# Performance work log

Hardware: AMD Instinct MI355X
Metric: run time of the kernel (lower is better)

The kernel has to match this reference:

```python
import jax, jax.numpy as jnp
import numpy as np

N = 131072   # total nodes in batch
E = 524288   # directed edges
B = 2048     # number of graphs
H = 128      # hidden_dim
NF = 30      # node_feature_dim
GF = 4415    # gene_feature_dim
L = 3        # gnn_layers
EPS = 1e-5   # batchnorm eps


def setup_inputs() -> dict:
    key = jax.random.key(0)
    ks = jax.random.split(key, 24)
    rn = lambda k, s, sc=0.05: jax.random.normal(k, s, jnp.float32) * sc
    return {
        "x": jax.random.normal(ks[0], (N, NF), jnp.float32),
        "gene_features": jax.random.normal(ks[1], (B, GF), jnp.float32),
        "edge_index": jax.random.randint(ks[2], (2, E), 0, N),
        "batch": (jnp.arange(N) * B) // N,  # sorted, every graph non-empty
        "W_emb": rn(ks[3], (NF, H)), "b_emb": jnp.zeros((H,), jnp.float32),
        "Wg": rn(ks[4], (L, H, H)), "bg": jnp.zeros((L, H), jnp.float32),
        "bn_gamma": jnp.ones((L, H), jnp.float32), "bn_beta": jnp.zeros((L, H), jnp.float32),
        "Wd1": rn(ks[5], (2 * H, H)), "bd1": jnp.zeros((H,), jnp.float32),
        "Wd2": rn(ks[6], (H, H)), "bd2": jnp.zeros((H,), jnp.float32),
        "Wge1": rn(ks[7], (GF, 256)), "bge1": jnp.zeros((256,), jnp.float32),
        "g_gamma": jnp.ones((256,), jnp.float32), "g_beta": jnp.zeros((256,), jnp.float32),
        "Wge2": rn(ks[8], (256, H)), "bge2": jnp.zeros((H,), jnp.float32),
        "Wh1": rn(ks[9], (2 * H, H)), "bh1": jnp.zeros((H,), jnp.float32),
        "h_gamma": jnp.ones((H,), jnp.float32), "h_beta": jnp.zeros((H,), jnp.float32),
        "Wh2": rn(ks[10], (H, 64)), "bh2": jnp.zeros((64,), jnp.float32),
        "Wh3": rn(ks[11], (64, 1)), "bh3": jnp.zeros((1,), jnp.float32),
    }


def _bn_eval(x, gamma, beta):
    # inference batchnorm with running_mean=0, running_var=1
    return x * (gamma / jnp.sqrt(1.0 + EPS)) + beta


def _gcn_conv(h, W, b, src, dst):
    # PyG GCNConv: add self-loops, symmetric deg normalization, W first, bias after agg
    hw = h @ W                                            # [N,H]
    loop = jnp.arange(N)
    src_a = jnp.concatenate([src, loop])                  # [E+N]
    dst_a = jnp.concatenate([dst, loop])
    deg = jax.ops.segment_sum(jnp.ones((E + N,), hw.dtype), dst_a, num_segments=N)
    dinv = jnp.where(deg > 0, jax.lax.rsqrt(deg), 0.0)
    norm = dinv[src_a] * dinv[dst_a]                      # [E+N]
    msgs = hw[src_a] * norm[:, None]                      # gather [E+N,H]
    out = jax.ops.segment_sum(msgs, dst_a, num_segments=N)
    return out + b


def reference(x, gene_features, edge_index, batch, W_emb, b_emb, Wg, bg, bn_gamma,
              bn_beta, Wd1, bd1, Wd2, bd2, Wge1, bge1, g_gamma, g_beta, Wge2, bge2,
              Wh1, bh1, h_gamma, h_beta, Wh2, bh2, Wh3, bh3):
    src, dst = edge_index[0], edge_index[1]
    h = jax.nn.relu(x @ W_emb + b_emb)                    # [N,H]
    for i in range(L):
        hn = _gcn_conv(h, Wg[i], bg[i], src, dst)
        hn = jax.nn.relu(_bn_eval(hn, bn_gamma[i], bn_beta[i]))
        h = hn if i == 0 else h + hn                      # residual for i>0
    # global mean / max pooling per graph
    counts = jax.ops.segment_sum(jnp.ones((N,), h.dtype), batch, num_segments=B)
    mean_pool = jax.ops.segment_sum(h, batch, num_segments=B) / jnp.maximum(counts, 1.0)[:, None]
    max_pool = jax.ops.segment_max(h, batch, num_segments=B)
    graph_repr = jnp.concatenate([mean_pool, max_pool], axis=1)   # [B,2H]
    drug = jax.nn.relu(graph_repr @ Wd1 + bd1) @ Wd2 + bd2        # [B,H]
    g1 = jax.nn.relu(_bn_eval(gene_features @ Wge1 + bge1, g_gamma, g_beta))
    gene = jax.nn.relu(g1 @ Wge2 + bge2)                          # [B,H]
    comb = jnp.concatenate([drug, gene], axis=1)                  # [B,2H]
    z = jax.nn.relu(_bn_eval(comb @ Wh1 + bh1, h_gamma, h_beta))
    z = jax.nn.relu(z @ Wh2 + bh2)
    return z @ Wh3 + bh3                                          # [B,1]
```

## Files before the change

kernel.cpp:

```cpp
#include <hip/hip_runtime.h>

#define N_NODES 131072
#define E_EDGES 524288
#define B_GR    2048
#define H_DIM   128
#define NF_DIM  30
#define GF_DIM  4415
#define GF_PAD  4416
#define BN_SCALE 0.9999950000374997f
#define NSPLIT  32

typedef __bf16 bf16x8 __attribute__((ext_vector_type(8)));
typedef float  f32x4  __attribute__((ext_vector_type(4)));
typedef unsigned int uint32;
typedef uint32 u32x4 __attribute__((ext_vector_type(4)));

__device__ __forceinline__ void split2(float x, __bf16& hi, __bf16& lo){
    hi = (__bf16)x;
    lo = (__bf16)(x - (float)hi);
}
__device__ __forceinline__ uint32 bfbits(float x){
    __bf16 h = (__bf16)x;
    return (uint32)__builtin_bit_cast(unsigned short, h);
}
__device__ __forceinline__ float unpack_even(uint32 u){ return __uint_as_float(u<<16); }
__device__ __forceinline__ float unpack_odd (uint32 u){ return __uint_as_float(u & 0xffff0000u); }
__device__ __forceinline__ uint32 pack2(float e, float o){ return bfbits(e) | (bfbits(o)<<16); }


__global__ void k_zero2(int* __restrict__ a, int na, float* __restrict__ b, int nb){
    int i = blockIdx.x*256 + threadIdx.x;
    if(i < na) a[i] = 0;
    int j = i - na;
    if(j >= 0 && j < nb) b[j] = 0.f;
}

__global__ void k_count(const int* __restrict__ dst, int* __restrict__ counts){
    int e = blockIdx.x*256 + threadIdx.x;
    if(e < E_EDGES) atomicAdd(&counts[dst[e]], 1);
}

__global__ void k_scan1(int* __restrict__ counts, int* __restrict__ bsums){
    __shared__ int s[1024];
    int t = threadIdx.x;
    int gi = blockIdx.x*1024 + t;
    int v = counts[gi];
    s[t] = v; __syncthreads();
    for(int off=1; off<1024; off<<=1){
        int x = (t>=off) ? s[t-off] : 0;
        __syncthreads();
        s[t] += x;
        __syncthreads();
    }
    counts[gi] = s[t] - v;
    if(t == 1023) bsums[blockIdx.x] = s[t];
}

__global__ void k_scan2(int* __restrict__ bsums){
    __shared__ int s[128];
    int t = threadIdx.x;
    int v = bsums[t]; s[t] = v; __syncthreads();
    for(int off=1; off<128; off<<=1){
        int x = (t>=off) ? s[t-off] : 0;
        __syncthreads();
        s[t] += x;
        __syncthreads();
    }
    bsums[t] = s[t] - v;
}

__global__ void k_scan3(const int* __restrict__ counts, const int* __restrict__ bsums,
                        int* __restrict__ rowptr, float* __restrict__ dinv,
                        int* __restrict__ cursor){
    int i = blockIdx.x*1024 + threadIdx.x;
    int r0 = counts[i] + bsums[blockIdx.x];
    int r1;
    if(i == N_NODES-1){
        r1 = E_EDGES;
        rowptr[N_NODES] = E_EDGES;
    } else {
        int ip = i + 1;
        int nb = (threadIdx.x == 1023) ? blockIdx.x + 1 : blockIdx.x;
        r1 = counts[ip] + bsums[nb];
    }
    rowptr[i] = r0;
    dinv[i] = rsqrtf((float)(r1 - r0) + 1.0f);
    cursor[i] = r0;
}

__global__ void k_fill(const int* __restrict__ src, const int* __restrict__ dst,
                       int* __restrict__ cursor, int* __restrict__ csr){
    int e = blockIdx.x*256 + threadIdx.x;
    if(e < E_EDGES){
        int p = atomicAdd(&cursor[dst[e]], 1);
        csr[p] = src[e];
    }
}


__global__ void k_split_weights(const float* __restrict__ Wge1, __bf16* __restrict__ wth,
                                __bf16* __restrict__ wtl,
                                const float* __restrict__ Wg, __bf16* __restrict__ gth,
                                __bf16* __restrict__ gtl,
                                const float* __restrict__ Wemb, __bf16* __restrict__ eth,
                                __bf16* __restrict__ etl){
    __shared__ float sTile[64][65];
    unsigned bid = blockIdx.x;
    int tid = threadIdx.x;
    if(bid < 276u){
        int kt = bid % 69u, ct = bid / 69u;
        int k0 = kt*64, c0 = ct*64;
        #pragma unroll
        for(int i=0;i<16;i++){
            int idx = i*256 + tid;
            int kk = idx >> 6, cc = idx & 63;
            int k = k0 + kk;
            sTile[kk][cc] = (k < GF_DIM) ? Wge1[(size_t)k*256 + c0 + cc] : 0.f;
        }
        __syncthreads();
        #pragma unroll
        for(int i=0;i<16;i++){
            int idx = i*256 + tid;
            int cc = idx >> 6, kk = idx & 63;
            float v = sTile[kk][cc];
            size_t o = (size_t)(c0 + cc)*GF_PAD + k0 + kk;
            split2(v, wth[o], wtl[o]);
        }
    } else if(bid < 276u + 192u){
        int idx = (bid - 276u)*256 + tid;
        int l = idx >> 14, i = idx & 16383;
        int k = i >> 7, c = i & 127;
        float v = Wg[idx];
        int o = (l << 14) + (c << 7) + k;
        split2(v, gth[o], gtl[o]);
    } else {
        int idx = (bid - 468u)*256 + tid;
        int c = idx >> 5, k = idx & 31;
        float v = (k < NF_DIM) ? Wemb[k*H_DIM + c] : 0.f;
        split2(v, eth[idx], etl[idx]);
    }
}


__global__ __launch_bounds__(256)
void k_emb_mfma(const float* __restrict__ x,
                const __bf16* __restrict__ wth, const __bf16* __restrict__ wtl,
                const float* __restrict__ bias, uint32* __restrict__ Hh2,
                uint32* __restrict__ Hl2){
    __shared__ float sT[4][32*68];
    int wave = threadIdx.x >> 6, lane = threadIdx.x & 63;
    int lr = lane & 15, lq = lane >> 4;
    int rbase = blockIdx.x*128 + wave*32;
    const f32x4 zero4 = {0.f,0.f,0.f,0.f};
    const float* xr0 = x + (size_t)(rbase + lr)*NF_DIM;
    const float* xr1 = x + (size_t)(rbase + 16 + lr)*NF_DIM;
    bf16x8 A0h, A0l, A1h, A1l;
    #pragma unroll
    for(int t=0;t<8;t++){
        int k = lq*8 + t;
        float v0 = (k < NF_DIM) ? xr0[k] : 0.f;
        float v1 = (k < NF_DIM) ? xr1[k] : 0.f;
        __bf16 h, l;
        split2(v0, h, l); A0h[t] = h; A0l[t] = l;
        split2(v1, h, l); A1h[t] = h; A1l[t] = l;
    }
    int orow = lane >> 3;
    int oq   = lane & 7;
    float* sW = sT[wave];
    for(int ph=0; ph<2; ph++){
        #pragma unroll
        for(int cc=0; cc<4; cc++){
            int col = (ph*4+cc)*16 + lr;
            bf16x8 Bh = *(const bf16x8*)(wth + col*32 + lq*8);
            bf16x8 Bl = *(const bf16x8*)(wtl + col*32 + lq*8);
            f32x4 a0 = zero4, a1 = zero4;
            a0 = __builtin_amdgcn_mfma_f32_16x16x32_bf16(A0h, Bh, a0, 0,0,0);
            a0 = __builtin_amdgcn_mfma_f32_16x16x32_bf16(A0l, Bh, a0, 0,0,0);
            a0 = __builtin_amdgcn_mfma_f32_16x16x32_bf16(A0h, Bl, a0, 0,0,0);
            a1 = __builtin_amdgcn_mfma_f32_16x16x32_bf16(A1h, Bh, a1, 0,0,0);
            a1 = __builtin_amdgcn_mfma_f32_16x16x32_bf16(A1l, Bh, a1, 0,0,0);
            a1 = __builtin_amdgcn_mfma_f32_16x16x32_bf16(A1h, Bl, a1, 0,0,0);
            #pragma unroll
            for(int r=0;r<4;r++){
                sW[(lq*4+r)*68 + cc*16 + lr]    = a0[r];
                sW[(16+lq*4+r)*68 + cc*16 + lr] = a1[r];
            }
        }
        __syncthreads();
        int cg = ph*64 + oq*8;
        float bb[8];
        *(float4*)&bb[0] = *(const float4*)(bias + cg);
        *(float4*)&bb[4] = *(const float4*)(bias + cg + 4);
        #pragma unroll
        for(int i=0;i<4;i++){
            int row = i*8 + orow;
            float v[8];
            *(float4*)&v[0] = *(float4*)&sW[row*68 + oq*8];
            *(float4*)&v[4] = *(float4*)&sW[row*68 + oq*8 + 4];
            uint32 oh[4], ol[4];
            #pragma unroll
            for(int p=0;p<4;p++){
                float ve = fmaxf(v[2*p]   + bb[2*p],   0.f);
                float vo = fmaxf(v[2*p+1] + bb[2*p+1], 0.f);
                uint32 he = bfbits(ve), ho = bfbits(vo);
                oh[p] = he | (ho<<16);
                float le = ve - __uint_as_float(he<<16);
                float lo = vo - __uint_as_float(ho<<16);
                ol[p] = pack2(le, lo);
            }
            size_t oidx = (size_t)(rbase + row)*64 + (cg>>1);
            *(uint4*)(Hh2 + oidx) = make_uint4(oh[0],oh[1],oh[2],oh[3]);
            *(uint4*)(Hl2 + oidx) = make_uint4(ol[0],ol[1],ol[2],ol[3]);
        }
        __syncthreads();
    }
}


struct MetaA {
    int   j0A, cA, j0B, cB;
    float dnA, dnB;
    uint32 shA, slA, shB, slB;
};

__device__ __forceinline__ void load_metaA(MetaA& m, int nA, int lane,
                                           const int* __restrict__ rowptr,
                                           const float* __restrict__ dinv,
                                           const uint32* __restrict__ Hh2,
                                           const uint32* __restrict__ Hl2){
    int nB = nA + 8;
    int a0 = rowptr[nA], a1 = rowptr[nA+1];
    int b0 = rowptr[nB], b1 = rowptr[nB+1];
    m.j0A = a0; m.cA = a1 - a0;
    m.j0B = b0; m.cB = b1 - b0;
    m.dnA = dinv[nA]; m.dnB = dinv[nB];
    size_t iA = (size_t)nA*64 + lane, iB = (size_t)nB*64 + lane;
    m.shA = Hh2[iA]; m.slA = Hl2[iA];
    m.shB = Hh2[iB]; m.slB = Hl2[iB];
}

__device__ __forceinline__ void load_jj(int* jjA, int* jjB, const MetaA& m,
                                        const int* __restrict__ csr){
    int jmA = m.j0A + m.cA - 1;
    int jmB = m.j0B + m.cB - 1;
    #pragma unroll
    for(int t=0;t<8;t++){
        int ia = m.j0A + t; ia = ia > jmA ? jmA : ia;
        int ib = m.j0B + t; ib = ib > jmB ? jmB : ib;
        jjA[t] = csr[ia] & (N_NODES-1);
        jjB[t] = csr[ib] & (N_NODES-1);
    }
}

__device__ __forceinline__ void agg_step(
        const MetaA& cur, const int* jjA, const int* jjB, int ii,
        MetaA* m2, int n2,
        int* jj1A, int* jj1B, const MetaA* m1,
        int base16, int lane,
        const uint32* __restrict__ Hh2, const uint32* __restrict__ Hl2,
        const float* __restrict__ dinv, const int* __restrict__ rowptr,
        const int* __restrict__ csr,
        uint32* __restrict__ AhL, uint32* __restrict__ AlL){
    uint32 rrA[8], rrB[8];
    float  wwA[8], wwB[8];
    #pragma unroll
    for(int t=0;t<8;t++){
        wwA[t] = (t < cur.cA) ? dinv[jjA[t]] : 0.f;
        rrA[t] = Hh2[(size_t)jjA[t]*64 + lane];
        wwB[t] = (t < cur.cB) ? dinv[jjB[t]] : 0.f;
        rrB[t] = Hh2[(size_t)jjB[t]*64 + lane];
    }
    if(m2) load_metaA(*m2, n2, lane, rowptr, dinv, Hh2, Hl2);
    if(m1) load_jj(jj1A, jj1B, *m1, csr);
    float axA = (unpack_even(cur.shA) + unpack_even(cur.slA)) * cur.dnA;
    float ayA = (unpack_odd(cur.shA)  + unpack_odd(cur.slA))  * cur.dnA;
    float axB = (unpack_even(cur.shB) + unpack_even(cur.slB)) * cur.dnB;
    float ayB = (unpack_odd(cur.shB)  + unpack_odd(cur.slB))  * cur.dnB;
    #pragma unroll
    for(int t=0;t<8;t++){
        axA = fmaf(unpack_even(rrA[t]), wwA[t], axA);
        ayA = fmaf(unpack_odd(rrA[t]),  wwA[t], ayA);
        axB = fmaf(unpack_even(rrB[t]), wwB[t], axB);
        ayB = fmaf(unpack_odd(rrB[t]),  wwB[t], ayB);
    }
    int nb = cur.cA > cur.cB ? cur.cA : cur.cB;
    if(nb > 8){
        int jmA = cur.j0A + cur.cA - 1;
        int jmB = cur.j0B + cur.cB - 1;
        for(int j=8; j<nb; j+=8){
            int jja[8], jjb[8]; float wa[8], wb[8]; uint32 ra[8], rb[8];
            #pragma unroll
            for(int t=0;t<8;t++){
                int ia = cur.j0A + j + t; ia = ia > jmA ? jmA : ia;
                int ib = cur.j0B + j + t; ib = ib > jmB ? jmB : ib;
                jja[t] = csr[ia] & (N_NODES-1);
                jjb[t] = csr[ib] & (N_NODES-1);
            }
            #pragma unroll
            for(int t=0;t<8;t++){
                wa[t] = (j + t < cur.cA) ? dinv[jja[t]] : 0.f;
                ra[t] = Hh2[(size_t)jja[t]*64 + lane];
                wb[t] = (j + t < cur.cB) ? dinv[jjb[t]] : 0.f;
                rb[t] = Hh2[(size_t)jjb[t]*64 + lane];
            }
            #pragma unroll
            for(int t=0;t<8;t++){
                axA = fmaf(unpack_even(ra[t]), wa[t], axA);
                ayA = fmaf(unpack_odd(ra[t]),  wa[t], ayA);
                axB = fmaf(unpack_even(rb[t]), wb[t], axB);
                ayB = fmaf(unpack_odd(rb[t]),  wb[t], ayB);
            }
        }
    }
    axA *= cur.dnA; ayA *= cur.dnA;
    axB *= cur.dnB; ayB *= cur.dnB;
    int rowA = base16 + ii, rowB = rowA + 8;
    uint32 hxA = bfbits(axA), hyA = bfbits(ayA);
    AhL[rowA*68 + lane] = hxA | (hyA<<16);
    AlL[rowA*68 + lane] = pack2(axA - __uint_as_float(hxA<<16),
                                ayA - __uint_as_float(hyA<<16));
    uint32 hxB = bfbits(axB), hyB = bfbits(ayB);
    AhL[rowB*68 + lane] = hxB | (hyB<<16);
    AlL[rowB*68 + lane] = pack2(axB - __uint_as_float(hxB<<16),
                                ayB - __uint_as_float(hyB<<16));
}

__global__ __launch_bounds__(512, 4)
void k_layer(const __bf16* __restrict__ curHh, const __bf16* __restrict__ curHl,
             const float* __restrict__ dinv, const int* __restrict__ rowptr,
             const int* __restrict__ csr,
             const __bf16* __restrict__ Bth, const __bf16* __restrict__ Btl,
             const float* __restrict__ bias, const float* __restrict__ gamma,
             const float* __restrict__ beta,
             uint32* __restrict__ outHh2, uint32* __restrict__ outHl2, int residual){
    __shared__ uint32 smem[8*32*68];
    uint32* AhL = smem;
    uint32* AlL = smem + 128*68;
    int tid  = threadIdx.x;
    int wave = __builtin_amdgcn_readfirstlane(tid >> 6);
    int lane = tid & 63;
    int rbase = blockIdx.x * 128;
    int base16 = wave*16;
    const uint32* Hh2 = (const uint32*)curHh;
    const uint32* Hl2 = (const uint32*)curHl;

    {
        MetaA m0, m1, m2;
        int jj0A[8], jj0B[8], jj1A[8], jj1B[8];
        int nb0 = rbase + base16;
        load_metaA(m0, nb0+0, lane, rowptr, dinv, Hh2, Hl2);
        load_metaA(m1, nb0+1, lane, rowptr, dinv, Hh2, Hl2);
        load_jj(jj0A, jj0B, m0, csr);
        agg_step(m0, jj0A, jj0B, 0, &m2, nb0+2, jj1A, jj1B, &m1,
                 base16, lane, Hh2, Hl2, dinv, rowptr, csr, AhL, AlL);
        agg_step(m1, jj1A, jj1B, 1, &m0, nb0+3, jj0A, jj0B, &m2,
                 base16, lane, Hh2, Hl2, dinv, rowptr, csr, AhL, AlL);
        agg_step(m2, jj0A, jj0B, 2, &m1, nb0+4, jj1A, jj1B, &m0,
                 base16, lane, Hh2, Hl2, dinv, rowptr, csr, AhL, AlL);
        agg_step(m0, jj1A, jj1B, 3, &m2, nb0+5, jj0A, jj0B, &m1,
                 base16, lane, Hh2, Hl2, dinv, rowptr, csr, AhL, AlL);
        agg_step(m1, jj0A, jj0B, 4, &m0, nb0+6, jj1A, jj1B, &m2,
                 base16, lane, Hh2, Hl2, dinv, rowptr, csr, AhL, AlL);
        agg_step(m2, jj1A, jj1B, 5, &m1, nb0+7, jj0A, jj0B, &m0,
                 base16, lane, Hh2, Hl2, dinv, rowptr, csr, AhL, AlL);
        agg_step(m0, jj0A, jj0B, 6, nullptr, 0, jj1A, jj1B, &m1,
                 base16, lane, Hh2, Hl2, dinv, rowptr, csr, AhL, AlL);
        agg_step(m1, jj1A, jj1B, 7, nullptr, 0, nullptr, nullptr, nullptr,
                 base16, lane, Hh2, Hl2, dinv, rowptr, csr, AhL, AlL);
    }
    __syncthreads();

    int lr = lane & 15, lq = lane >> 4;
    int wr = wave & 3, wc = wave >> 2;
    int r0 = wr*32;
    bf16x8 A0h[4], A0l[4], A1h[4], A1l[4];
    #pragma unroll
    for(int ks=0;ks<4;ks++){
        int u0 = (r0 + lr)*68 + lq*4 + ks*16;
        int u1 = (r0 + 16 + lr)*68 + lq*4 + ks*16;
        A0h[ks] = __builtin_bit_cast(bf16x8, *(const u32x4*)(AhL + u0));
        A0l[ks] = __builtin_bit_cast(bf16x8, *(const u32x4*)(AlL + u0));
        A1h[ks] = __builtin_bit_cast(bf16x8, *(const u32x4*)(AhL + u1));
        A1l[ks] = __builtin_bit_cast(bf16x8, *(const u32x4*)(AlL + u1));
    }
    __syncthreads();

    float* stg = (float*)smem + wave*(32*68);
    const f32x4 zero4 = {0.f,0.f,0.f,0.f};
    #pragma unroll
    for(int cc=0; cc<4; cc++){
        int col = wc*64 + cc*16 + lr;
        f32x4 a0 = zero4, a1 = zero4;
        #pragma unroll
        for(int ks=0;ks<4;ks++){
            bf16x8 Bh = *(const bf16x8*)(Bth + col*H_DIM + ks*32 + lq*8);
            bf16x8 Bl = *(const bf16x8*)(Btl + col*H_DIM + ks*32 + lq*8);
            a0 = __builtin_amdgcn_mfma_f32_16x16x32_bf16(A0h[ks], Bh, a0, 0,0,0);
            a0 = __builtin_amdgcn_mfma_f32_16x16x32_bf16(A0l[ks], Bh, a0, 0,0,0);
            a0 = __builtin_amdgcn_mfma_f32_16x16x32_bf16(A0h[ks], Bl, a0, 0,0,0);
            a1 = __builtin_amdgcn_mfma_f32_16x16x32_bf16(A1h[ks], Bh, a1, 0,0,0);
            a1 = __builtin_amdgcn_mfma_f32_16x16x32_bf16(A1l[ks], Bh, a1, 0,0,0);
            a1 = __builtin_amdgcn_mfma_f32_16x16x32_bf16(A1h[ks], Bl, a1, 0,0,0);
        }
        #pragma unroll
        for(int r=0;r<4;r++){
            stg[(lq*4+r)*68 + cc*16 + lr]    = a0[r];
            stg[(16+lq*4+r)*68 + cc*16 + lr] = a1[r];
        }
    }

    int orow = lane >> 3;
    int oq   = lane & 7;
    int cg = wc*64 + oq*8;
    float bb[8], gg[8], tt[8];
    *(float4*)&bb[0] = *(const float4*)(bias + cg);
    *(float4*)&bb[4] = *(const float4*)(bias + cg + 4);
    *(float4*)&gg[0] = *(const float4*)(gamma + cg);
    *(float4*)&gg[4] = *(const float4*)(gamma + cg + 4);
    *(float4*)&tt[0] = *(const float4*)(beta + cg);
    *(float4*)&tt[4] = *(const float4*)(beta + cg + 4);
    #pragma unroll
    for(int p=0;p<8;p++) gg[p] *= BN_SCALE;
    #pragma unroll
    for(int i=0;i<4;i++){
        int row = i*8 + orow;
        float v[8];
        *(float4*)&v[0] = *(float4*)&stg[row*68 + oq*8];
        *(float4*)&v[4] = *(float4*)&stg[row*68 + oq*8 + 4];
        size_t oidx = (size_t)(rbase + r0 + row)*64 + (cg>>1);
        uint4 oldh = {0,0,0,0}, oldl = {0,0,0,0};
        if(residual){
            oldh = *(const uint4*)(Hh2 + oidx);
            oldl = *(const uint4*)(Hl2 + oidx);
        }
        uint32 ohv[4] = {oldh.x,oldh.y,oldh.z,oldh.w};
        uint32 olv[4] = {oldl.x,oldl.y,oldl.z,oldl.w};
        uint32 oh[4], ol[4];
        #pragma unroll
        for(int p=0;p<4;p++){
            float ve = fmaxf(fmaf(v[2*p]   + bb[2*p],   gg[2*p],   tt[2*p]),   0.f);
            float vo = fmaxf(fmaf(v[2*p+1] + bb[2*p+1], gg[2*p+1], tt[2*p+1]), 0.f);
            if(residual){
                ve += unpack_even(ohv[p]) + unpack_even(olv[p]);
                vo += unpack_odd(ohv[p])  + unpack_odd(olv[p]);
            }
            uint32 he = bfbits(ve), ho = bfbits(vo);
            oh[p] = he | (ho<<16);
            float le = ve - __uint_as_float(he<<16);
            float lo = vo - __uint_as_float(ho<<16);
            ol[p] = pack2(le, lo);
        }
        *(uint4*)(outHh2 + oidx) = make_uint4(oh[0],oh[1],oh[2],oh[3]);
        *(uint4*)(outHl2 + oidx) = make_uint4(ol[0],ol[1],ol[2],ol[3]);
    }
}


__global__ __launch_bounds__(256)
void k_gemm_gf_mfma(const float* __restrict__ Agf,
                    const __bf16* __restrict__ Bth, const __bf16* __restrict__ Btl,
                    float* __restrict__ g1acc){
    int rt = blockIdx.x & 31;
    int sp = blockIdx.x >> 5;
    int ks0 = (sp*138) >> 5, ks1 = ((sp+1)*138) >> 5;
    int wave = threadIdx.x >> 6, lane = threadIdx.x & 63;
    int lr = lane & 15, lq = lane >> 4;
    int rbase = rt*64 + (wave & 1)*32;
    int cbase = (wave >> 1)*128;
    const f32x4 zero4 = {0.f,0.f,0.f,0.f};
    f32x4 acc[8][2];
    #pragma unroll
    for(int ct=0;ct<8;ct++){ acc[ct][0] = zero4; acc[ct][1] = zero4; }
    for(int ks=ks0; ks<ks1; ks++){
        int kc = ks*32;
        const float* ar0 = Agf + (size_t)(rbase + lr)*GF_DIM + kc + lq*8;
        const float* ar1 = ar0 + (size_t)16*GF_DIM;
        bf16x8 A0h, A0l, A1h, A1l;
        if(kc + 32 <= GF_DIM){
            #pragma unroll
            for(int t=0;t<8;t++){
                __bf16 h, l;
                split2(ar0[t], h, l); A0h[t] = h; A0l[t] = l;
                split2(ar1[t], h, l); A1h[t] = h; A1l[t] = l;
            }
        } else {
            #pragma unroll
            for(int t=0;t<8;t++){
                int k = kc + lq*8 + t;
                float v0 = 0.f, v1 = 0.f;
                if(k < GF_DIM){ v0 = ar0[t]; v1 = ar1[t]; }
                __bf16 h, l;
                split2(v0, h, l); A0h[t] = h; A0l[t] = l;
                split2(v1, h, l); A1h[t] = h; A1l[t] = l;
            }
        }
        #pragma unroll
        for(int ct=0;ct<8;ct++){
            size_t bo = (size_t)(cbase + ct*16 + lr)*GF_PAD + kc + lq*8;
            bf16x8 Bh = *(const bf16x8*)(Bth + bo);
            bf16x8 Bl = *(const bf16x8*)(Btl + bo);
            acc[ct][0] = __builtin_amdgcn_mfma_f32_16x16x32_bf16(A0h, Bh, acc[ct][0], 0,0,0);
            acc[ct][0] = __builtin_amdgcn_mfma_f32_16x16x32_bf16(A0l, Bh, acc[ct][0], 0,0,0);
            acc[ct][0] = __builtin_amdgcn_mfma_f32_16x16x32_bf16(A0h, Bl, acc[ct][0], 0,0,0);
            acc[ct][1] = __builtin_amdgcn_mfma_f32_16x16x32_bf16(A1h, Bh, acc[ct][1], 0,0,0);
            acc[ct][1] = __builtin_amdgcn_mfma_f32_16x16x32_bf16(A1l, Bh, acc[ct][1], 0,0,0);
            acc[ct][1] = __builtin_amdgcn_mfma_f32_16x16x32_bf16(A1h, Bl, acc[ct][1], 0,0,0);
        }
    }
    #pragma unroll
    for(int ct=0;ct<8;ct++)
        #pragma unroll
        for(int s=0;s<2;s++)
            #pragma unroll
            for(int r=0;r<4;r++)
                atomicAdd(&g1acc[(size_t)(rbase + s*16 + lq*4 + r)*256 + cbase + ct*16 + lr],
                          acc[ct][s][r]);
}


__device__ __forceinline__ void load_w4(const float* __restrict__ W, int off, int tid,
                                        float4* t){
    const float4* s = (const float4*)(W + off);
    t[0] = s[tid];
    t[1] = s[tid + 512];
    t[2] = s[tid + 1024];
    t[3] = s[tid + 1536];
}
__device__ __forceinline__ void write_w4(float* sW, int tid, const float4* t){
    float4* d = (float4*)sW;
    d[tid]        = t[0];
    d[tid + 512]  = t[1];
    d[tid + 1024] = t[2];
    d[tid + 1536] = t[3];
}

__device__ __forceinline__ void dense_stage128(
        const float* __restrict__ W, int nck, const float* sA, int lda,
        float* sO, int ldo, float* sW, int tid, int c, int ga, int gb,
        float bias_c, float gsc, float bsh, int do_relu){
    float4 t[4];
    load_w4(W, 0, tid, t);
    write_w4(sW, tid, t);
    __syncthreads();
    float a0 = bias_c, a1 = bias_c;
    for(int ck=0; ck<nck; ck++){
        if(ck+1 < nck) load_w4(W, (ck+1)*8192, tid, t);
        const float* aga = sA + ga*lda + ck*64;
        const float* agb = sA + gb*lda + ck*64;
        #pragma unroll
        for(int k=0;k<64;k++){
            float w = sW[k*128 + c];
            a0 = fmaf(aga[k], w, a0);
            a1 = fmaf(agb[k], w, a1);
        }
        __syncthreads();
        if(ck+1 < nck){ write_w4(sW, tid, t); __syncthreads(); }
    }
    a0 = fmaf(a0, gsc, bsh);
    a1 = fmaf(a1, gsc, bsh);
    if(do_relu){ a0 = fmaxf(a0, 0.f); a1 = fmaxf(a1, 0.f); }
    sO[ga*ldo + c] = a0;
    sO[gb*ldo + c] = a1;
}

__global__ __launch_bounds__(512)
void k_head(const uint32* __restrict__ Hh2, const uint32* __restrict__ Hl2,
            const float* __restrict__ g1acc,
            const float* __restrict__ bge1, const float* __restrict__ g_g,
            const float* __restrict__ g_b,
            const float* __restrict__ Wd1, const float* __restrict__ bd1,
            const float* __restrict__ Wd2, const float* __restrict__ bd2,
            const float* __restrict__ Wge2, const float* __restrict__ bge2,
            const float* __restrict__ Wh1, const float* __restrict__ bh1,
            const float* __restrict__ h_g, const float* __restrict__ h_b,
            const float* __restrict__ Wh2, const float* __restrict__ bh2,
            const float* __restrict__ Wh3, const float* __restrict__ bh3,
            float* __restrict__ out){
    __shared__ float sPool[8][256];
    __shared__ float sG1[8][256];
    __shared__ float sT1[8][128];
    __shared__ float sComb[8][256];
    __shared__ float sZ[8][128];
    __shared__ float sZ2[8][64];
    __shared__ float sW[8192];
    int tid = threadIdx.x;
    int wave = tid >> 6, lane = tid & 63;
    int g0 = blockIdx.x*8;
    {
        int idx = tid*4;
        int g = idx >> 8, c = idx & 255;
        float4 a  = *(const float4*)&g1acc[(size_t)(g0+g)*256 + c];
        float4 b  = *(const float4*)&bge1[c];
        float4 gm = *(const float4*)&g_g[c];
        float4 bt = *(const float4*)&g_b[c];
        sG1[g][c+0] = fmaxf(fmaf(a.x + b.x, gm.x*BN_SCALE, bt.x), 0.f);
        sG1[g][c+1] = fmaxf(fmaf(a.y + b.y, gm.y*BN_SCALE, bt.y), 0.f);
        sG1[g][c+2] = fmaxf(fmaf(a.z + b.z, gm.z*BN_SCALE, bt.z), 0.f);
        sG1[g][c+3] = fmaxf(fmaf(a.w + b.w, gm.w*BN_SCALE, bt.w), 0.f);
    }
    {
        size_t base = (size_t)(g0+wave)*4096 + lane;
        float se = 0.f, so = 0.f, me = -3.4e38f, mo = -3.4e38f;
        #pragma unroll 8
        for(int r=0;r<64;r++){
            uint32 h = Hh2[base + r*64];
            uint32 l = Hl2[base + r*64];
            float ve = unpack_even(h) + unpack_even(l);
            float vo = unpack_odd(h)  + unpack_odd(l);
            se += ve; so += vo;
            me = fmaxf(me, ve); mo = fmaxf(mo, vo);
        }
        sPool[wave][2*lane]       = se*(1.f/64.f);
        sPool[wave][2*lane+1]     = so*(1.f/64.f);
        sPool[wave][128+2*lane]   = me;
        sPool[wave][128+2*lane+1] = mo;
    }
    __syncthreads();
    int c = tid & 127, q = tid >> 7;
    int ga = 2*q, gb = 2*q + 1;
    dense_stage128(Wd1, 4, &sPool[0][0], 256, &sT1[0][0], 128, sW, tid, c, ga, gb,
                   bd1[c], 1.f, 0.f, 1);
    dense_stage128(Wd2, 2, &sT1[0][0], 128, &sComb[0][0], 256, sW, tid, c, ga, gb,
                   bd2[c], 1.f, 0.f, 0);
    dense_stage128(Wge2, 4, &sG1[0][0], 256, &sComb[0][0] + 128, 256, sW, tid, c, ga, gb,
                   bge2[c], 1.f, 0.f, 1);
    dense_stage128(Wh1, 4, &sComb[0][0], 256, &sZ[0][0], 128, sW, tid, c, ga, gb,
                   bh1[c], h_g[c]*BN_SCALE, h_b[c], 1);
    {
        float4 t[4];
        load_w4(Wh2, 0, tid, t);
        write_w4(sW, tid, t);
        __syncthreads();
        int c2 = tid & 63, q2 = tid >> 6;
        float a = bh2[c2];
        #pragma unroll
        for(int k=0;k<128;k++)
            a = fmaf(sZ[q2][k], sW[k*64 + c2], a);
        sZ2[q2][c2] = fmaxf(a, 0.f);
    }
    __syncthreads();
    {
        float v = sZ2[wave][lane] * Wh3[lane];
        #pragma unroll
        for(int off=32; off; off>>=1) v += __shfl_down(v, off);
        if(lane == 0) out[g0 + wave] = v + bh3[0];
    }
}


extern "C" void kernel_launch(void* const* d_in, const int* in_sizes, int n_in,
                              void* d_out, int out_size, void* d_ws, size_t ws_size,
                              hipStream_t stream){
    (void)in_sizes; (void)n_in; (void)out_size; (void)ws_size;
    const float* x    = (const float*)d_in[0];
    const float* gf   = (const float*)d_in[1];
    const int*   ei   = (const int*)  d_in[2];
    const float* W_emb= (const float*)d_in[4];
    const float* b_emb= (const float*)d_in[5];
    const float* Wg   = (const float*)d_in[6];
    const float* bg   = (const float*)d_in[7];
    const float* bn_g = (const float*)d_in[8];
    const float* bn_b = (const float*)d_in[9];
    const float* Wd1  = (const float*)d_in[10];
    const float* bd1  = (const float*)d_in[11];
    const float* Wd2  = (const float*)d_in[12];
    const float* bd2  = (const float*)d_in[13];
    const float* Wge1 = (const float*)d_in[14];
    const float* bge1 = (const float*)d_in[15];
    const float* g_g  = (const float*)d_in[16];
    const float* g_b  = (const float*)d_in[17];
    const float* Wge2 = (const float*)d_in[18];
    const float* bge2 = (const float*)d_in[19];
    const float* Wh1  = (const float*)d_in[20];
    const float* bh1  = (const float*)d_in[21];
    const float* h_g  = (const float*)d_in[22];
    const float* h_b  = (const float*)d_in[23];
    const float* Wh2  = (const float*)d_in[24];
    const float* bh2  = (const float*)d_in[25];
    const float* Wh3  = (const float*)d_in[26];
    const float* bh3  = (const float*)d_in[27];
    float* outp = (float*)d_out;

    char* base = (char*)d_ws;
    __bf16* Hh = (__bf16*)base;
    __bf16* Hl = (__bf16*)(base + (32u<<20));
    __bf16* Ph = (__bf16*)(base + (64u<<20));
    __bf16* Pl = (__bf16*)(base + (96u<<20));
    __bf16* wge_th = (__bf16*)(base + (64u<<20));
    __bf16* wge_tl = (__bf16*)(base + (64u<<20) + 2260992);
    char* T = base + (128u<<20);
    float* g1acc = (float*)T;
    int* counts = (int*)(g1acc + B_GR*256);
    int* rowptr = counts + N_NODES;
    int* cursor = rowptr + (N_NODES+1);
    int* csr    = cursor + N_NODES;
    int* bsums  = csr + E_EDGES;
    float* dinv = (float*)(bsums + 128);
    __bf16* wg_th = (__bf16*)(dinv + N_NODES);
    __bf16* wg_tl = wg_th + 3*16384;
    __bf16* we_th = wg_tl + 3*16384;
    __bf16* we_tl = we_th + 128*32;

    const int* src = ei;
    const int* dst = ei + E_EDGES;

    k_split_weights<<<484, 256, 0, stream>>>(Wge1, wge_th, wge_tl, Wg, wg_th, wg_tl,
                                             W_emb, we_th, we_tl);

    k_zero2<<<(N_NODES + B_GR*256 + 255)/256, 256, 0, stream>>>(counts, N_NODES,
                                                                g1acc, B_GR*256);

    k_gemm_gf_mfma<<<32*NSPLIT, 256, 0, stream>>>(gf, wge_th, wge_tl, g1acc);

    k_count<<<E_EDGES/256, 256, 0, stream>>>(dst, counts);
    k_scan1<<<128, 1024, 0, stream>>>(counts, bsums);
    k_scan2<<<1, 128, 0, stream>>>(bsums);
    k_scan3<<<128, 1024, 0, stream>>>(counts, bsums, rowptr, dinv, cursor);
    k_fill <<<E_EDGES/256, 256, 0, stream>>>(src, dst, cursor, csr);

    k_emb_mfma<<<N_NODES/128, 256, 0, stream>>>(x, we_th, we_tl, b_emb,
                                                (uint32*)Hh, (uint32*)Hl);

    uint32 *curh = (uint32*)Hh, *curl = (uint32*)Hl;
    uint32 *outh = (uint32*)Ph, *outl = (uint32*)Pl;
    for(int i=0;i<3;i++){
        k_layer<<<N_NODES/128, 512, 0, stream>>>((const __bf16*)curh, (const __bf16*)curl,
                                                 dinv, rowptr, csr,
                                                 wg_th + i*16384, wg_tl + i*16384,
                                                 bg + i*H_DIM, bn_g + i*H_DIM, bn_b + i*H_DIM,
                                                 outh, outl, i > 0);
        uint32* th = curh; curh = outh; outh = th;
        uint32* tl = curl; curl = outl; outl = tl;
    }

    k_head<<<B_GR/8, 512, 0, stream>>>(curh, curl, g1acc, bge1, g_g, g_b,
                                       Wd1, bd1, Wd2, bd2, Wge2, bge2,
                                       Wh1, bh1, h_g, h_b, Wh2, bh2, Wh3, bh3, outp);
}
```

Before: 583.0 us.

## Tile Wge1 weights per MFMA block, stage A via LDS, replace atomics with split-K reduce

The transposed, split Wge1 weights are repacked into contiguous 16x32 tiles, one per MFMA fragment, so B loads are dense. The gene-feature A tile is now loaded with coalesced float4 reads into shared memory before the bf16 split. Each split-K slice writes its partials to a scratch buffer, and a separate reduce kernel sums them, which replaces the float atomics and the zeroing of g1acc. The split count is halved to 16, which lowers reduce traffic but leaves fewer blocks in flight and adds a kernel launch.

Measured after the change: 582.8 us (median of 2 runs). Within noise of the previous version (-0.0%).

```diff
diff --git a/kernel.cpp b/kernel.cpp
--- a/kernel.cpp
+++ b/kernel.cpp
@@ -8,7 +8,7 @@
 #define GF_DIM  4415
 #define GF_PAD  4416
 #define BN_SCALE 0.9999950000374997f
-#define NSPLIT  32
+#define NSPLIT  16
 
 typedef __bf16 bf16x8 __attribute__((ext_vector_type(8)));
 typedef float  f32x4  __attribute__((ext_vector_type(4)));
@@ -28,11 +28,9 @@
 __device__ __forceinline__ uint32 pack2(float e, float o){ return bfbits(e) | (bfbits(o)<<16); }
 
 
-__global__ void k_zero2(int* __restrict__ a, int na, float* __restrict__ b, int nb){
+__global__ void k_zero_int(int* __restrict__ p, int n){
     int i = blockIdx.x*256 + threadIdx.x;
-    if(i < na) a[i] = 0;
-    int j = i - na;
-    if(j >= 0 && j < nb) b[j] = 0.f;
+    if(i < n) p[i] = 0;
 }
 
 __global__ void k_count(const int* __restrict__ dst, int* __restrict__ counts){
@@ -123,7 +121,8 @@
             int idx = i*256 + tid;
             int cc = idx >> 6, kk = idx & 63;
             float v = sTile[kk][cc];
-            size_t o = (size_t)(c0 + cc)*GF_PAD + k0 + kk;
+            int c = c0 + cc, k = k0 + kk;
+            size_t o = ((size_t)(c >> 4)*138 + (k >> 5))*512 + (c & 15)*32 + (k & 31);
             split2(v, wth[o], wtl[o]);
         }
     } else if(bid < 276u + 192u){
@@ -459,44 +458,54 @@
 __global__ __launch_bounds__(256)
 void k_gemm_gf_mfma(const float* __restrict__ Agf,
                     const __bf16* __restrict__ Bth, const __bf16* __restrict__ Btl,
-                    float* __restrict__ g1acc){
+                    float* __restrict__ gpart){
+    __shared__ float sA[64*34];
     int rt = blockIdx.x & 31;
     int sp = blockIdx.x >> 5;
-    int ks0 = (sp*138) >> 5, ks1 = ((sp+1)*138) >> 5;
-    int wave = threadIdx.x >> 6, lane = threadIdx.x & 63;
+    int ks0 = (sp*138) >> 4, ks1 = ((sp+1)*138) >> 4;
+    int tid = threadIdx.x;
+    int wave = tid >> 6, lane = tid & 63;
     int lr = lane & 15, lq = lane >> 4;
-    int rbase = rt*64 + (wave & 1)*32;
+    int rblk = rt*64;
+    int rhalf = (wave & 1)*32;
     int cbase = (wave >> 1)*128;
     const f32x4 zero4 = {0.f,0.f,0.f,0.f};
     f32x4 acc[8][2];
     #pragma unroll
     for(int ct=0;ct<8;ct++){ acc[ct][0] = zero4; acc[ct][1] = zero4; }
+    int srow = tid >> 2, sq = tid & 3;
     for(int ks=ks0; ks<ks1; ks++){
         int kc = ks*32;
-        const float* ar0 = Agf + (size_t)(rbase + lr)*GF_DIM + kc + lq*8;
-        const float* ar1 = ar0 + (size_t)16*GF_DIM;
+        __syncthreads();
+        {
+            int k0 = kc + sq*8;
+            const float* srcp = Agf + (size_t)(rblk + srow)*GF_DIM + k0;
+            float v[8];
+            if(k0 + 8 <= GF_DIM){
+                *(float4*)&v[0] = *(const float4*)srcp;
+                *(float4*)&v[4] = *(const float4*)(srcp + 4);
+            } else {
+                #pragma unroll
+                for(int t=0;t<8;t++) v[t] = (k0 + t < GF_DIM) ? srcp[t] : 0.f;
+            }
+            #pragma unroll
+            for(int t=0;t<8;t++) sA[srow*34 + sq*8 + t] = v[t];
+        }
+        __syncthreads();
         bf16x8 A0h, A0l, A1h, A1l;
-        if(kc + 32 <= GF_DIM){
+        {
+            const float* a0p = &sA[(rhalf + lr)*34 + lq*8];
+            const float* a1p = &sA[(rhalf + 16 + lr)*34 + lq*8];
             #pragma unroll
             for(int t=0;t<8;t++){
                 __bf16 h, l;
-                split2(ar0[t], h, l); A0h[t] = h; A0l[t] = l;
-                split2(ar1[t], h, l); A1h[t] = h; A1l[t] = l;
+                split2(a0p[t], h, l); A0h[t] = h; A0l[t] = l;
+                split2(a1p[t], h, l); A1h[t] = h; A1l[t] = l;
             }
-        } else {
-            #pragma unroll
-            for(int t=0;t<8;t++){
-                int k = kc + lq*8 + t;
-                float v0 = 0.f, v1 = 0.f;
-                if(k < GF_DIM){ v0 = ar0[t]; v1 = ar1[t]; }
-                __bf16 h, l;
-                split2(v0, h, l); A0h[t] = h; A0l[t] = l;
-                split2(v1, h, l); A1h[t] = h; A1l[t] = l;
-            }
         }
         #pragma unroll
         for(int ct=0;ct<8;ct++){
-            size_t bo = (size_t)(cbase + ct*16 + lr)*GF_PAD + kc + lq*8;
+            size_t bo = ((size_t)((cbase >> 4) + ct)*138 + ks)*512 + lr*32 + lq*8;
             bf16x8 Bh = *(const bf16x8*)(Bth + bo);
             bf16x8 Bl = *(const bf16x8*)(Btl + bo);
             acc[ct][0] = __builtin_amdgcn_mfma_f32_16x16x32_bf16(A0h, Bh, acc[ct][0], 0,0,0);
@@ -507,14 +516,22 @@
             acc[ct][1] = __builtin_amdgcn_mfma_f32_16x16x32_bf16(A1h, Bl, acc[ct][1], 0,0,0);
         }
     }
+    float* po = gpart + (size_t)sp*(B_GR*256);
     #pragma unroll
     for(int ct=0;ct<8;ct++)
         #pragma unroll
         for(int s=0;s<2;s++)
             #pragma unroll
             for(int r=0;r<4;r++)
-                atomicAdd(&g1acc[(size_t)(rbase + s*16 + lq*4 + r)*256 + cbase + ct*16 + lr],
-                          acc[ct][s][r]);
+                po[(size_t)(rblk + rhalf + s*16 + lq*4 + r)*256 + cbase + ct*16 + lr] = acc[ct][s][r];
+}
+
+__global__ void k_gene_reduce(const float* __restrict__ gpart, float* __restrict__ g1acc){
+    int i = blockIdx.x*256 + threadIdx.x;
+    float v = 0.f;
+    #pragma unroll 8
+    for(int sp=0;sp<NSPLIT;sp++) v += gpart[(size_t)sp*(B_GR*256) + i];
+    g1acc[i] = v;
 }
 
 
@@ -686,6 +703,7 @@
     __bf16* Hl = (__bf16*)(base + (32u<<20));
     __bf16* Ph = (__bf16*)(base + (64u<<20));
     __bf16* Pl = (__bf16*)(base + (96u<<20));
+    float*  gpart  = (float*)base;
     __bf16* wge_th = (__bf16*)(base + (64u<<20));
     __bf16* wge_tl = (__bf16*)(base + (64u<<20) + 2260992);
     char* T = base + (128u<<20);
@@ -707,11 +725,10 @@
     k_split_weights<<<484, 256, 0, stream>>>(Wge1, wge_th, wge_tl, Wg, wg_th, wg_tl,
                                              W_emb, we_th, we_tl);
 
-    k_zero2<<<(N_NODES + B_GR*256 + 255)/256, 256, 0, stream>>>(counts, N_NODES,
-                                                                g1acc, B_GR*256);
-
-    k_gemm_gf_mfma<<<32*NSPLIT, 256, 0, stream>>>(gf, wge_th, wge_tl, g1acc);
-
+    k_gemm_gf_mfma<<<32*NSPLIT, 256, 0, stream>>>(gf, wge_th, wge_tl, gpart);
+    k_gene_reduce <<<(B_GR*256)/256, 256, 0, stream>>>(gpart, g1acc);
+
+    k_zero_int<<<N_NODES/256, 256, 0, stream>>>(counts, N_NODES);
     k_count<<<E_EDGES/256, 256, 0, stream>>>(dst, counts);
     k_scan1<<<128, 1024, 0, stream>>>(counts, bsums);
     k_scan2<<<1, 128, 0, stream>>>(bsums);
```
